# Kernel optimization log

Hardware: AMD Instinct MI355X
Metric: run time of the kernel (lower is better)

## Reference

```python
import jax, jax.numpy as jnp
import numpy as np

B, H, W, C = 32, 56, 56, 192
P, HEADS = 7, 6
HD = C // HEADS
SCALE = HD ** -0.5
EPS = 1e-5


def _rel_pos_index(p):
    coords = np.stack(np.meshgrid(np.arange(p), np.arange(p), indexing='ij')).reshape(2, -1)
    rel = (coords[:, :, None] - coords[:, None, :]).transpose(1, 2, 0).astype(np.int64)
    rel[:, :, 0] += p - 1
    rel[:, :, 1] += p - 1
    rel[:, :, 0] *= 2 * p - 1
    return rel.sum(-1)  # (p*p, p*p)

REL_IDX = jnp.asarray(_rel_pos_index(P))


def _ln(x, g, b):
    mu = x.mean(-1, keepdims=True)
    var = ((x - mu) ** 2).mean(-1, keepdims=True)
    return (x - mu) * jax.lax.rsqrt(var + EPS) * g + b


def setup_inputs():
    key = jax.random.key(0)
    ks = jax.random.split(key, 8)
    s = 0.02
    return {
        'x': jax.random.normal(ks[0], (B, H * W, C), jnp.float32),
        'norm1_g': jnp.ones((C,), jnp.float32),
        'norm1_b': jnp.zeros((C,), jnp.float32),
        'qkv_w': jax.random.normal(ks[1], (C, 3 * C), jnp.float32) * s,
        'qkv_b': jnp.zeros((3 * C,), jnp.float32),
        'rpe_table': jax.random.normal(ks[2], ((2 * P - 1) ** 2, HEADS), jnp.float32) * s,
        'proj_w': jax.random.normal(ks[3], (C, C), jnp.float32) * s,
        'proj_b': jnp.zeros((C,), jnp.float32),
        'norm2_g': jnp.ones((C,), jnp.float32),
        'norm2_b': jnp.zeros((C,), jnp.float32),
        'fc1_w': jax.random.normal(ks[4], (C, 4 * C), jnp.float32) * s,
        'fc1_b': jnp.zeros((4 * C,), jnp.float32),
        'fc2_w': jax.random.normal(ks[5], (4 * C, C), jnp.float32) * s,
        'fc2_b': jnp.zeros((C,), jnp.float32),
    }


def reference(x, norm1_g, norm1_b, qkv_w, qkv_b, rpe_table, proj_w, proj_b,
              norm2_g, norm2_b, fc1_w, fc1_b, fc2_w, fc2_b):
    N = P * P
    shortcut = x
    h = _ln(x, norm1_g, norm1_b).reshape(B, H, W, C)
    # partition -> (B*nH*nW, N, C)
    h = h.reshape(B, H // P, P, W // P, P, C).transpose(0, 1, 3, 2, 4, 5)
    patches = h.reshape(-1, N, C)
    B_ = patches.shape[0]
    # qkv
    qkv = (patches @ qkv_w + qkv_b).reshape(B_, N, 3, HEADS, HD)
    q, k, v = qkv[:, :, 0], qkv[:, :, 1], qkv[:, :, 2]  # (B_, N, HEADS, HD)
    attn = jnp.einsum('bnhd,bmhd->bhnm', q * SCALE, k)
    bias = rpe_table[REL_IDX.reshape(-1)].reshape(N, N, HEADS).transpose(2, 0, 1)
    attn = jax.nn.softmax(attn + bias[None], axis=-1)
    out = jnp.einsum('bhnm,bmhd->bnhd', attn, v).reshape(B_, N, C)
    out = out @ proj_w + proj_b
    # reverse -> (B, H*W, C)
    out = out.reshape(B, H // P, W // P, P, P, C).transpose(0, 1, 3, 2, 4, 5).reshape(B, H * W, C)
    x = shortcut + out
    h = _ln(x, norm2_g, norm2_b)
    h = jax.nn.gelu(h @ fc1_w + fc1_b, approximate=False) @ fc2_w + fc2_b
    return x + h
```

## Files before the change

kernel.cpp:

```cpp
#include <hip/hip_runtime.h>
#include <cstdint>

using u16 = unsigned short;
using u32 = unsigned int;

typedef __bf16 bf16x8 __attribute__((ext_vector_type(8)));
typedef float f32x4 __attribute__((ext_vector_type(4)));
typedef short short4v __attribute__((ext_vector_type(4)));

constexpr int TOK = 100352;
constexpr float LOG2E = 1.4426950408889634f;
constexpr float SCALE_QL = 0.25503490f;

__device__ __forceinline__ float bf2f(u16 u) {
  union { u32 i; float f; } z; z.i = ((u32)u) << 16; return z.f;
}
__device__ __forceinline__ u16 f2bf(float f) {
  union { float f; u32 i; } z; z.f = f;
  u32 r = z.i + 0x7FFFu + ((z.i >> 16) & 1u);
  return (u16)(r >> 16);
}
__device__ __forceinline__ u32 pk2bf(float a, float b) {
  union { __bf16 h[2]; u32 w; } z;
  z.h[0] = (__bf16)a; z.h[1] = (__bf16)b; return z.w;
}

__device__ __forceinline__ float gelu_f(float v) {
  float t = -v * (2.3022587f + 0.10294455f * v * v);
  float e = exp2f(t);
  return v * __builtin_amdgcn_rcpf(1.f + e);
}

__device__ __forceinline__ void gload_lds16(const void* g, void* l) {
  __builtin_amdgcn_global_load_lds((const __attribute__((address_space(1))) void*)g,
                                   (__attribute__((address_space(3))) void*)l, 16, 0, 0);
}

__global__ __launch_bounds__(256) void prep_weights(
    const float* __restrict__ qkv_w, const float* __restrict__ proj_w,
    const float* __restrict__ fc1_w, const float* __restrict__ fc2_w,
    u16* __restrict__ qkvT, u16* __restrict__ projT,
    u16* __restrict__ fc1T, u16* __restrict__ fc2T)
{
  int id = blockIdx.x * 256 + threadIdx.x;
  if (id < 122880) {
    int n = id / 192, k = id - n * 192;
    float v = (n < 576) ? qkv_w[(size_t)k * 576 + n] : 0.f;
    qkvT[id] = f2bf(v);
  } else if (id < 172032) {
    int t = id - 122880;
    int n = t / 192, k = t - n * 192;
    float v = (n < 192) ? proj_w[(size_t)k * 192 + n] : 0.f;
    projT[t] = f2bf(v);
  } else if (id < 319488) {
    int t = id - 172032;
    int n = t / 192, k = t - n * 192;
    int sg = (k >> 3) ^ (n & 7);
    fc1T[n * 192 + sg * 8 + (k & 7)] = f2bf(fc1_w[(size_t)k * 768 + n]);
  } else if (id < 466944) {
    int t = id - 319488;
    int oc = t / 768, gc = t - oc * 768;
    int ch = gc >> 5, gcl = gc & 31;
    int f = gcl >> 4, gq = (gcl >> 2) & 3, e = gcl & 3;
    int P = oc * 4 + (gq ^ ((oc >> 2) & 3));
    fc2T[ch * 6144 + P * 8 + f * 4 + e] = f2bf(fc2_w[(size_t)gc * 192 + oc]);
  }
}

__global__ __launch_bounds__(256) void ln_kernel(const float* __restrict__ x,
                                                 const float* __restrict__ g,
                                                 const float* __restrict__ b,
                                                 u16* __restrict__ out) {
  int row  = blockIdx.x * 4 + (threadIdx.x >> 6);
  int lane = threadIdx.x & 63;
  const float* xr = x + (size_t)row * 192;
  float v[3];
  #pragma unroll
  for (int t = 0; t < 3; ++t) v[t] = xr[lane + 64 * t];
  float s = v[0] + v[1] + v[2];
  #pragma unroll
  for (int o = 32; o; o >>= 1) s += __shfl_xor(s, o);
  float mu = s * (1.f / 192.f);
  float q = 0.f;
  #pragma unroll
  for (int t = 0; t < 3; ++t) { float d = v[t] - mu; q += d * d; }
  #pragma unroll
  for (int o = 32; o; o >>= 1) q += __shfl_xor(q, o);
  float rs = rsqrtf(q * (1.f / 192.f) + 1e-5f);
  #pragma unroll
  for (int t = 0; t < 3; ++t) {
    int c = lane + 64 * t;
    out[(size_t)row * 192 + c] = f2bf((v[t] - mu) * rs * g[c] + b[c]);
  }
}

enum { MQKV = 0 };

template<int MODE, int MT, int NT, int N, int K, int LDC>
__global__ __launch_bounds__(256) void gemm_kernel(
    const u16* __restrict__ A, const u16* __restrict__ BT,
    const float* __restrict__ bias,
    u16* __restrict__ outb)
{
  constexpr int NWG = MT * NT;
  constexpr int NTL = K / 32;
  __shared__ __align__(16) u16 As[3][4096];
  __shared__ __align__(16) u16 Bs[3][4096];
  int tid = threadIdx.x;
  int wg = blockIdx.x;
  int lin = (wg & 7) * (NWG / 8) + (wg >> 3);
  int tileM = (lin / NT) * 128, tileN = (lin % NT) * 128;
  int lane = tid & 63, wave = tid >> 6;
  int wm = wave >> 1, wn = wave & 1;
  int g = lane >> 4, l15 = lane & 15;
  f32x4 acc[4][4] = {};

  int r0 = tid >> 2, kc = (tid & 3) * 8;
  const u16* Arow0 = A  + (size_t)(tileM + r0)      * K + kc;
  const u16* Arow1 = A  + (size_t)(tileM + r0 + 64) * K + kc;
  const u16* Brow0 = BT + (size_t)(tileN + r0)      * K + kc;
  const u16* Brow1 = BT + (size_t)(tileN + r0 + 64) * K + kc;
  const int wo = wave * 512;

#define GSTAGE(buf, k0) do {                              \
    gload_lds16(Arow0 + (k0), &As[buf][wo]);              \
    gload_lds16(Arow1 + (k0), &As[buf][2048 + wo]);       \
    gload_lds16(Brow0 + (k0), &Bs[buf][wo]);              \
    gload_lds16(Brow1 + (k0), &Bs[buf][2048 + wo]);       \
  } while (0)

  GSTAGE(0, 0);
  GSTAGE(1, 32);

  #pragma unroll
  for (int t = 0; t < NTL; ++t) {
    if (t + 1 < NTL) asm volatile("s_waitcnt vmcnt(4)" ::: "memory");
    else             asm volatile("s_waitcnt vmcnt(0)" ::: "memory");
    __builtin_amdgcn_s_barrier();
    __builtin_amdgcn_sched_barrier(0);
    if (t + 2 < NTL) GSTAGE((t + 2) % 3, (t + 2) * 32);
    const int cur = t % 3;
    bf16x8 af[4], bfr[4];
    #pragma unroll
    for (int mi = 0; mi < 4; ++mi)
      af[mi] = *(const bf16x8*)&As[cur][(wm * 64 + mi * 16 + l15) * 32 + g * 8];
    #pragma unroll
    for (int ni = 0; ni < 4; ++ni)
      bfr[ni] = *(const bf16x8*)&Bs[cur][(wn * 64 + ni * 16 + l15) * 32 + g * 8];
    #pragma unroll
    for (int mi = 0; mi < 4; ++mi)
      #pragma unroll
      for (int ni = 0; ni < 4; ++ni)
        acc[mi][ni] = __builtin_amdgcn_mfma_f32_16x16x32_bf16(bfr[ni], af[mi], acc[mi][ni], 0, 0, 0);
    __builtin_amdgcn_sched_barrier(0);
  }
#undef GSTAGE

  int cb = tileN + wn * 64 + g * 4;
  f32x4 bv4[4];
  bool cok[4];
  #pragma unroll
  for (int ni = 0; ni < 4; ++ni) {
    cok[ni] = (cb + ni * 16) < N;
    bv4[ni] = cok[ni] ? *(const f32x4*)&bias[cb + ni * 16] : f32x4{};
  }
  #pragma unroll
  for (int mi = 0; mi < 4; ++mi) {
    size_t row = (size_t)(tileM + wm * 64 + mi * 16 + l15);
    u16* orow = outb + row * LDC + cb;
    #pragma unroll
    for (int ni = 0; ni < 4; ++ni) {
      if (!cok[ni]) continue;
      float v0 = acc[mi][ni][0] + bv4[ni][0];
      float v1 = acc[mi][ni][1] + bv4[ni][1];
      float v2 = acc[mi][ni][2] + bv4[ni][2];
      float v3 = acc[mi][ni][3] + bv4[ni][3];
      if (MODE == MQKV && (cb + ni * 16) < 192) {
        v0 *= SCALE_QL; v1 *= SCALE_QL; v2 *= SCALE_QL; v3 *= SCALE_QL;
      }
      uint2 w;
      w.x = pk2bf(v0, v1);
      w.y = pk2bf(v2, v3);
      *(uint2*)&orow[ni * 16] = w;
    }
  }
}

__global__ __launch_bounds__(256, 2) void proj_ln(
    const u16* __restrict__ A,
    const u16* __restrict__ BT,
    const float* __restrict__ bias,
    const float* __restrict__ x,
    const float* __restrict__ n2g, const float* __restrict__ n2b,
    float* __restrict__ resid, u16* __restrict__ h2)
{
  constexpr int NWG = 784;
  __shared__ __align__(16) u16 As[3][4096];
  __shared__ __align__(16) u16 Bs[3][6144];
  int tid = threadIdx.x;
  int wg = blockIdx.x;
  int lin = (wg & 7) * (NWG / 8) + (wg >> 3);
  int tileM = lin * 128;
  int lane = tid & 63, wave = tid >> 6;
  int g = lane >> 4, l15 = lane & 15;
  f32x4 acc[2][12] = {};

  int r0 = tid >> 2, kc = (tid & 3) * 8;
  const u16* Arow0 = A + (size_t)(tileM + r0)      * 192 + kc;
  const u16* Arow1 = A + (size_t)(tileM + r0 + 64) * 192 + kc;
  const u16* Brow[3];
  #pragma unroll
  for (int i = 0; i < 3; ++i) {
    int s = (wave * 3 + i) * 64 + lane;
    Brow[i] = BT + (size_t)(s >> 2) * 192 + (s & 3) * 8;
  }
  const int wo = wave * 512;

#define PSTAGE(buf, k0) do {                                   \
    gload_lds16(Arow0 + (k0), &As[buf][wo]);                   \
    gload_lds16(Arow1 + (k0), &As[buf][2048 + wo]);            \
    _Pragma("unroll")                                          \
    for (int i = 0; i < 3; ++i)                                \
      gload_lds16(Brow[i] + (k0), &Bs[buf][(wave * 3 + i) * 512]); \
  } while (0)

  PSTAGE(0, 0);
  PSTAGE(1, 32);

  #pragma unroll
  for (int t = 0; t < 6; ++t) {
    if (t + 1 < 6) asm volatile("s_waitcnt vmcnt(5)" ::: "memory");
    else           asm volatile("s_waitcnt vmcnt(0)" ::: "memory");
    __builtin_amdgcn_s_barrier();
    __builtin_amdgcn_sched_barrier(0);
    if (t + 2 < 6) PSTAGE((t + 2) % 3, (t + 2) * 32);
    const int cur = t % 3;
    bf16x8 af[2], bfr[12];
    #pragma unroll
    for (int mi = 0; mi < 2; ++mi)
      af[mi] = *(const bf16x8*)&As[cur][(wave * 32 + mi * 16 + l15) * 32 + g * 8];
    #pragma unroll
    for (int ni = 0; ni < 12; ++ni)
      bfr[ni] = *(const bf16x8*)&Bs[cur][(ni * 16 + l15) * 32 + g * 8];
    #pragma unroll
    for (int mi = 0; mi < 2; ++mi)
      #pragma unroll
      for (int ni = 0; ni < 12; ++ni)
        acc[mi][ni] = __builtin_amdgcn_mfma_f32_16x16x32_bf16(bfr[ni], af[mi], acc[mi][ni], 0, 0, 0);
    __builtin_amdgcn_sched_barrier(0);
  }
#undef PSTAGE

  float s1[2] = {0.f, 0.f}, s2[2] = {0.f, 0.f};
  #pragma unroll
  for (int mi = 0; mi < 2; ++mi) {
    size_t row = (size_t)(tileM + wave * 32 + mi * 16 + l15);
    #pragma unroll
    for (int ni = 0; ni < 12; ++ni) {
      int cb = ni * 16 + g * 4;
      f32x4 bv = *(const f32x4*)&bias[cb];
      f32x4 xv = *(const f32x4*)&x[row * 192 + cb];
      f32x4 o;
      #pragma unroll
      for (int r = 0; r < 4; ++r) {
        o[r] = acc[mi][ni][r] + bv[r] + xv[r];
        s1[mi] += o[r];
        s2[mi] += o[r] * o[r];
      }
      acc[mi][ni] = o;
      *(f32x4*)&resid[row * 192 + cb] = o;
    }
  }
  #pragma unroll
  for (int mi = 0; mi < 2; ++mi) {
    s1[mi] += __shfl_xor(s1[mi], 16); s1[mi] += __shfl_xor(s1[mi], 32);
    s2[mi] += __shfl_xor(s2[mi], 16); s2[mi] += __shfl_xor(s2[mi], 32);
  }
  #pragma unroll
  for (int mi = 0; mi < 2; ++mi) {
    float mu = s1[mi] * (1.f / 192.f);
    float var = s2[mi] * (1.f / 192.f) - mu * mu;
    float rs = rsqrtf(var + 1e-5f);
    size_t row = (size_t)(tileM + wave * 32 + mi * 16 + l15);
    #pragma unroll
    for (int ni = 0; ni < 12; ++ni) {
      int cb = ni * 16 + g * 4;
      f32x4 gv = *(const f32x4*)&n2g[cb];
      f32x4 bv = *(const f32x4*)&n2b[cb];
      uint2 w;
      w.x = pk2bf((acc[mi][ni][0] - mu) * rs * gv[0] + bv[0],
                  (acc[mi][ni][1] - mu) * rs * gv[1] + bv[1]);
      w.y = pk2bf((acc[mi][ni][2] - mu) * rs * gv[2] + bv[2],
                  (acc[mi][ni][3] - mu) * rs * gv[3] + bv[3]);
      *(uint2*)&h2[row * 192 + cb] = w;
    }
  }
}

__global__ __launch_bounds__(256, 3) void mlp_fused(
    const u16* __restrict__ h2, const float* __restrict__ resid,
    const u16* __restrict__ w1g,
    const u16* __restrict__ w2g,
    const float* __restrict__ fc1b, const float* __restrict__ fc2b,
    float* __restrict__ out)
{
  __shared__ __align__(16) u16 W1c[2][6144];
  __shared__ __align__(16) u16 W2c[2][6144];
  __shared__ float B1s[768];
  __shared__ float B2s[192];

  int tid = threadIdx.x, lane = tid & 63, wave = tid >> 6;
  int g = lane >> 4, l15 = lane & 15;
  size_t row = (size_t)blockIdx.x * 64 + wave * 16 + l15;

  for (int c = tid; c < 768; c += 256) B1s[c] = fc1b[c];
  if (tid < 192) B2s[tid] = fc2b[tid];

  bf16x8 xf[6];
  #pragma unroll
  for (int ks = 0; ks < 6; ++ks)
    xf[ks] = *(const bf16x8*)&h2[row * 192 + ks * 32 + g * 8];

#define MSTAGE(c) do {                                                    \
    _Pragma("unroll")                                                     \
    for (int it = 0; it < 3; ++it) {                                      \
      int s = it * 256 + tid;                                             \
      gload_lds16(w1g + (size_t)(c) * 6144 + s * 8,                       \
                  &W1c[(c) & 1][(it * 256 + wave * 64) * 8]);             \
      gload_lds16(w2g + (size_t)(c) * 6144 + s * 8,                       \
                  &W2c[(c) & 1][(it * 256 + wave * 64) * 8]);             \
    }                                                                     \
  } while (0)

  MSTAGE(0);
  __syncthreads();

  f32x4 accO[12] = {};
  const int p2sw = g ^ ((l15 >> 2) & 3);

  #pragma unroll 2
  for (int c = 0; c < 24; ++c) {
    asm volatile("s_waitcnt vmcnt(0)" ::: "memory");
    __builtin_amdgcn_s_barrier();
    __builtin_amdgcn_sched_barrier(0);
    if (c + 1 < 24) MSTAGE(c + 1);
    const int bs = c & 1;

    f32x4 acc1[2] = {};
    #pragma unroll
    for (int ks = 0; ks < 6; ++ks) {
      #pragma unroll
      for (int f = 0; f < 2; ++f) {
        int rl = f * 16 + l15;
        int sg = (ks * 4 + g) ^ (rl & 7);
        bf16x8 wf = *(const bf16x8*)&W1c[bs][rl * 192 + sg * 8];
        acc1[f] = __builtin_amdgcn_mfma_f32_16x16x32_bf16(wf, xf[ks], acc1[f], 0, 0, 0);
      }
    }
    short4v bp[2];
    #pragma unroll
    for (int f = 0; f < 2; ++f) {
      f32x4 bv = *(const f32x4*)&B1s[c * 32 + f * 16 + g * 4];
      float p0 = gelu_f(acc1[f][0] + bv[0]);
      float p1 = gelu_f(acc1[f][1] + bv[1]);
      float p2 = gelu_f(acc1[f][2] + bv[2]);
      float p3 = gelu_f(acc1[f][3] + bv[3]);
      union { u32 w[2]; short4v v; } uu;
      uu.w[0] = pk2bf(p0, p1);
      uu.w[1] = pk2bf(p2, p3);
      bp[f] = uu.v;
    }
    #pragma unroll
    for (int n = 0; n < 12; ++n) {
      int oc = n * 16 + l15;
      int P = oc * 4 + p2sw;
      union { bf16x8 v8; short4v h[2]; } wu;
      wu.v8 = *(const bf16x8*)&W2c[bs][P * 8];
      accO[n] = __builtin_amdgcn_mfma_f32_16x16x16bf16_1k(wu.h[0], bp[0], accO[n], 0, 0, 0);
      accO[n] = __builtin_amdgcn_mfma_f32_16x16x16bf16_1k(wu.h[1], bp[1], accO[n], 0, 0, 0);
    }
    __builtin_amdgcn_sched_barrier(0);
  }
#undef MSTAGE

  const float* rrow = resid + row * 192;
  float*      orow = out + row * 192;
  #pragma unroll
  for (int n = 0; n < 12; ++n) {
    int cb = n * 16 + g * 4;
    f32x4 bv = *(const f32x4*)&B2s[cb];
    f32x4 rv = *(const f32x4*)&rrow[cb];
    f32x4 o;
    o[0] = accO[n][0] + bv[0] + rv[0];
    o[1] = accO[n][1] + bv[1] + rv[1];
    o[2] = accO[n][2] + bv[2] + rv[2];
    o[3] = accO[n][3] + bv[3] + rv[3];
    *(f32x4*)&orow[cb] = o;
  }
}

__global__ __launch_bounds__(384, 4) void attn_kernel(const u16* __restrict__ qkv,
                                                      const float* __restrict__ rpe,
                                                      u16* __restrict__ aout) {
  __shared__ __align__(16) u16 VT[192 * 72];
  __shared__ float RPE[1014];

  int tid = threadIdx.x;
  int win = blockIdx.x;
  int b = win >> 6, rem = win & 63, wh = rem >> 3, ww = rem & 7;
  const size_t wbase = (size_t)b * 3136 + (size_t)(wh * 7) * 56 + ww * 7;

  for (int c = tid; c < 1176; c += 384) {
    int dchunk = c / 49, tkn = c - dchunk * 49;
    int d0 = dchunk * 8;
    int yi = tkn / 7, xi = tkn - yi * 7;
    size_t t = wbase + yi * 56 + xi;
    uint4 v = *(const uint4*)&qkv[t * 576 + 384 + d0];
    const u16* e = (const u16*)&v;
    #pragma unroll
    for (int u = 0; u < 8; ++u) VT[(d0 + u) * 72 + tkn] = e[u];
  }
  for (int c = tid; c < 2880; c += 384) {
    int d = c / 15, n = 49 + (c - d * 15);
    VT[d * 72 + n] = 0;
  }
  for (int c = tid; c < 1014; c += 384) RPE[c] = rpe[c] * LOG2E;
  __syncthreads();

  int wave = tid >> 6, lane = tid & 63;
  int g = lane >> 4, l15 = lane & 15;
  int h = wave;

  bf16x8 afk[4], bfq[4];
  #pragma unroll
  for (int f = 0; f < 4; ++f) {
    int row = f * 16 + l15; row = min(row, 48);
    int y = row / 7, xx = row - y * 7;
    const u16* base = &qkv[(wbase + (size_t)y * 56 + xx) * 576];
    bfq[f] = *(const bf16x8*)(base + h * 32 + g * 8);
    afk[f] = *(const bf16x8*)(base + 192 + h * 32 + g * 8);
  }

  f32x4 acc[4][4] = {};
  __builtin_amdgcn_s_setprio(1);
  #pragma unroll
  for (int mj = 0; mj < 4; ++mj)
    #pragma unroll
    for (int ni = 0; ni < 4; ++ni)
      acc[mj][ni] = __builtin_amdgcn_mfma_f32_16x16x32_bf16(afk[mj], bfq[ni], acc[mj][ni], 0, 0, 0);
  __builtin_amdgcn_s_setprio(0);

  float sums[4];
  short4v bp[4][4];
  #pragma unroll
  for (int ni = 0; ni < 4; ++ni) {
    int i = ni * 16 + l15;
    int yi = i / 7, xi = i - yi * 7;
    #pragma unroll
    for (int mj = 0; mj < 4; ++mj)
      #pragma unroll
      for (int r = 0; r < 4; ++r) {
        int j = mj * 16 + g * 4 + r;
        int yj = j / 7, xj = j - yj * 7;
        int idx = (yi - yj + 6) * 13 + (xi - xj + 6);
        idx = max(0, min(idx, 168));
        float s = acc[mj][ni][r] + RPE[idx * 6 + h];
        acc[mj][ni][r] = (j < 49) ? s : -1e30f;
      }
    float m = -1e30f;
    #pragma unroll
    for (int mj = 0; mj < 4; ++mj) {
      f32x4 a = acc[mj][ni];
      m = fmaxf(m, fmaxf(fmaxf(a[0], a[1]), fmaxf(a[2], a[3])));
    }
    m = fmaxf(m, __shfl_xor(m, 16));
    m = fmaxf(m, __shfl_xor(m, 32));
    float sum = 0.f;
    #pragma unroll
    for (int mj = 0; mj < 4; ++mj) {
      float p0 = exp2f(acc[mj][ni][0] - m);
      float p1 = exp2f(acc[mj][ni][1] - m);
      float p2 = exp2f(acc[mj][ni][2] - m);
      float p3 = exp2f(acc[mj][ni][3] - m);
      sum += (p0 + p1) + (p2 + p3);
      union { u32 w[2]; short4v v; } uu;
      uu.w[0] = pk2bf(p0, p1);
      uu.w[1] = pk2bf(p2, p3);
      bp[ni][mj] = uu.v;
    }
    sum += __shfl_xor(sum, 16);
    sum += __shfl_xor(sum, 32);
    sums[ni] = sum;
  }

  f32x4 accO[2][4] = {};
  #pragma unroll
  for (int ks = 0; ks < 4; ++ks) {
    short4v av[2];
    #pragma unroll
    for (int md = 0; md < 2; ++md)
      av[md] = *(const short4v*)&VT[(h * 32 + md * 16 + l15) * 72 + ks * 16 + g * 4];
    __builtin_amdgcn_s_setprio(1);
    #pragma unroll
    for (int md = 0; md < 2; ++md)
      #pragma unroll
      for (int ni = 0; ni < 4; ++ni)
        accO[md][ni] = __builtin_amdgcn_mfma_f32_16x16x16bf16_1k(av[md], bp[ni][ks], accO[md][ni], 0, 0, 0);
    __builtin_amdgcn_s_setprio(0);
  }

  #pragma unroll
  for (int ni = 0; ni < 4; ++ni) {
    int i = ni * 16 + l15;
    if (i >= 49) continue;
    float inv = __builtin_amdgcn_rcpf(sums[ni]);
    int y = i / 7, xx = i - y * 7;
    u16* orow = &aout[(wbase + (size_t)y * 56 + xx) * 192 + h * 32];
    #pragma unroll
    for (int md = 0; md < 2; ++md) {
      int d0 = md * 16 + g * 4;
      *(u32*)&orow[d0]     = pk2bf(accO[md][ni][0] * inv, accO[md][ni][1] * inv);
      *(u32*)&orow[d0 + 2] = pk2bf(accO[md][ni][2] * inv, accO[md][ni][3] * inv);
    }
  }
}

extern "C" void kernel_launch(void* const* d_in, const int* in_sizes, int n_in,
                              void* d_out, int out_size, void* d_ws, size_t ws_size,
                              hipStream_t stream) {
  const float* x      = (const float*)d_in[0];
  const float* n1g    = (const float*)d_in[1];
  const float* n1b    = (const float*)d_in[2];
  const float* qkv_w  = (const float*)d_in[3];
  const float* qkv_b  = (const float*)d_in[4];
  const float* rpe    = (const float*)d_in[5];
  const float* proj_w = (const float*)d_in[6];
  const float* proj_b = (const float*)d_in[7];
  const float* n2g    = (const float*)d_in[8];
  const float* n2b    = (const float*)d_in[9];
  const float* fc1_w  = (const float*)d_in[10];
  const float* fc1_b  = (const float*)d_in[11];
  const float* fc2_w  = (const float*)d_in[12];
  const float* fc2_b  = (const float*)d_in[13];
  float* out = (float*)d_out;
  char* ws = (char*)d_ws;

  u16* qkvT  = (u16*)(ws + 0);
  u16* projT = (u16*)(ws + 245760);
  u16* fc1T  = (u16*)(ws + 344064);
  u16* fc2T  = (u16*)(ws + 638976);
  u16* ln1   = (u16*)(ws + 1048576);
  u16* qkvB  = (u16*)(ws + 39583744);
  float* resid = (float*)(ws + 78118912);
  u16* attnO = ln1;
  u16* h2    = qkvB;
  if (ws_size < 193724416u) return;

  prep_weights<<<1824, 256, 0, stream>>>(qkv_w, proj_w, fc1_w, fc2_w,
                                         qkvT, projT, fc1T, fc2T);

  ln_kernel<<<TOK/4, 256, 0, stream>>>(x, n1g, n1b, ln1);

  gemm_kernel<MQKV, 784, 5, 576, 192, 576><<<3920, 256, 0, stream>>>(
      ln1, qkvT, qkv_b, qkvB);

  attn_kernel<<<2048, 384, 0, stream>>>(qkvB, rpe, attnO);

  proj_ln<<<784, 256, 0, stream>>>(
      attnO, projT, proj_b, x, n2g, n2b, resid, h2);

  mlp_fused<<<TOK/64, 256, 0, stream>>>(
      h2, resid, fc1T, fc2T, fc1_b, fc2_b, out);
}
```

Before: 332.9 us.

## Retile QKV GEMM to 128x64 tiles with full-K B resident and per-wave A pipelining

Replaces the generic 128x128 QKV GEMM with a specialized kernel using 128x64 output tiles (9 N-tiles exactly covering 576, so no padded waste like 5x128=640). The whole 64x192 weight slice is loaded into LDS once, and each wave streams its own 32-row A slice through a private triple buffer, so the per-k-step block barriers go away. This is meant to cut wasted MFMA work on padded columns and barrier stalls. In exchange it launches more workgroups and A tiles are re-read across 9 N-tiles instead of 5.

Result: slower. 351.1 us (+5.5%).

```diff
diff --git a/kernel.cpp b/kernel.cpp
--- a/kernel.cpp
+++ b/kernel.cpp
@@ -94,88 +94,83 @@
   }
 }
 
-enum { MQKV = 0 };
-
-template<int MODE, int MT, int NT, int N, int K, int LDC>
-__global__ __launch_bounds__(256) void gemm_kernel(
+__global__ __launch_bounds__(256) void qkv_kernel(
     const u16* __restrict__ A, const u16* __restrict__ BT,
     const float* __restrict__ bias,
     u16* __restrict__ outb)
 {
-  constexpr int NWG = MT * NT;
-  constexpr int NTL = K / 32;
-  __shared__ __align__(16) u16 As[3][4096];
-  __shared__ __align__(16) u16 Bs[3][4096];
+  constexpr int NWG = 7056;
+  __shared__ __align__(16) u16 LDS[24576];
+  u16* Bl = LDS + 12288;
+
   int tid = threadIdx.x;
   int wg = blockIdx.x;
   int lin = (wg & 7) * (NWG / 8) + (wg >> 3);
-  int tileM = (lin / NT) * 128, tileN = (lin % NT) * 128;
+  int tileM = (lin / 9) * 128, tileN = (lin % 9) * 64;
   int lane = tid & 63, wave = tid >> 6;
-  int wm = wave >> 1, wn = wave & 1;
   int g = lane >> 4, l15 = lane & 15;
-  f32x4 acc[4][4] = {};
-
-  int r0 = tid >> 2, kc = (tid & 3) * 8;
-  const u16* Arow0 = A  + (size_t)(tileM + r0)      * K + kc;
-  const u16* Arow1 = A  + (size_t)(tileM + r0 + 64) * K + kc;
-  const u16* Brow0 = BT + (size_t)(tileN + r0)      * K + kc;
-  const u16* Brow1 = BT + (size_t)(tileN + r0 + 64) * K + kc;
-  const int wo = wave * 512;
-
-#define GSTAGE(buf, k0) do {                              \
-    gload_lds16(Arow0 + (k0), &As[buf][wo]);              \
-    gload_lds16(Arow1 + (k0), &As[buf][2048 + wo]);       \
-    gload_lds16(Brow0 + (k0), &Bs[buf][wo]);              \
-    gload_lds16(Brow1 + (k0), &Bs[buf][2048 + wo]);       \
+  f32x4 acc[2][4] = {};
+
+  #pragma unroll
+  for (int rnd = 0; rnd < 6; ++rnd) {
+    int s = rnd * 256 + tid;
+    int c = s >> 6, n = s & 63;
+    gload_lds16(BT + (size_t)(tileN + n) * 192 + c * 8, &Bl[(rnd * 256 + wave * 64) * 8]);
+  }
+  const u16* Arow = A + (size_t)(tileM + wave * 32) * 192;
+#define ASTAGE(t) do {                                                        \
+    const int b_ = (t) % 3;                                                   \
+    _Pragma("unroll")                                                         \
+    for (int i_ = 0; i_ < 2; ++i_) {                                          \
+      int s_ = i_ * 64 + lane;                                                \
+      gload_lds16(Arow + (size_t)(s_ & 31) * 192 + (t) * 32 + (s_ >> 5) * 8,  \
+                  &LDS[((wave * 3 + b_) * 128 + i_ * 64) * 8]);               \
+    }                                                                         \
   } while (0)
 
-  GSTAGE(0, 0);
-  GSTAGE(1, 32);
-
-  #pragma unroll
-  for (int t = 0; t < NTL; ++t) {
-    if (t + 1 < NTL) asm volatile("s_waitcnt vmcnt(4)" ::: "memory");
-    else             asm volatile("s_waitcnt vmcnt(0)" ::: "memory");
-    __builtin_amdgcn_s_barrier();
+  ASTAGE(0);
+  ASTAGE(1);
+  __syncthreads();
+
+  int cb = tileN + g * 4;
+  f32x4 bv4[4];
+  #pragma unroll
+  for (int ni = 0; ni < 4; ++ni) bv4[ni] = *(const f32x4*)&bias[cb + ni * 16];
+
+  #pragma unroll
+  for (int t = 0; t < 6; ++t) {
+    if (t + 2 < 6) ASTAGE(t + 2);
+    if (t < 4)      asm volatile("s_waitcnt vmcnt(4)" ::: "memory");
+    else if (t == 4) asm volatile("s_waitcnt vmcnt(2)" ::: "memory");
+    else            asm volatile("s_waitcnt vmcnt(0)" ::: "memory");
     __builtin_amdgcn_sched_barrier(0);
-    if (t + 2 < NTL) GSTAGE((t + 2) % 3, (t + 2) * 32);
-    const int cur = t % 3;
-    bf16x8 af[4], bfr[4];
-    #pragma unroll
-    for (int mi = 0; mi < 4; ++mi)
-      af[mi] = *(const bf16x8*)&As[cur][(wm * 64 + mi * 16 + l15) * 32 + g * 8];
+    const int buf = t % 3;
+    bf16x8 af[2], bfr[4];
+    #pragma unroll
+    for (int mi = 0; mi < 2; ++mi)
+      af[mi] = *(const bf16x8*)&LDS[((wave * 3 + buf) * 128 + g * 32 + mi * 16 + l15) * 8];
     #pragma unroll
     for (int ni = 0; ni < 4; ++ni)
-      bfr[ni] = *(const bf16x8*)&Bs[cur][(wn * 64 + ni * 16 + l15) * 32 + g * 8];
-    #pragma unroll
-    for (int mi = 0; mi < 4; ++mi)
+      bfr[ni] = *(const bf16x8*)&Bl[((t * 4 + g) * 64 + ni * 16 + l15) * 8];
+    #pragma unroll
+    for (int mi = 0; mi < 2; ++mi)
       #pragma unroll
       for (int ni = 0; ni < 4; ++ni)
         acc[mi][ni] = __builtin_amdgcn_mfma_f32_16x16x32_bf16(bfr[ni], af[mi], acc[mi][ni], 0, 0, 0);
-    __builtin_amdgcn_sched_barrier(0);
-  }
-#undef GSTAGE
-
-  int cb = tileN + wn * 64 + g * 4;
-  f32x4 bv4[4];
-  bool cok[4];
-  #pragma unroll
-  for (int ni = 0; ni < 4; ++ni) {
-    cok[ni] = (cb + ni * 16) < N;
-    bv4[ni] = cok[ni] ? *(const f32x4*)&bias[cb + ni * 16] : f32x4{};
-  }
-  #pragma unroll
-  for (int mi = 0; mi < 4; ++mi) {
-    size_t row = (size_t)(tileM + wm * 64 + mi * 16 + l15);
-    u16* orow = outb + row * LDC + cb;
+  }
+#undef ASTAGE
+
+  #pragma unroll
+  for (int mi = 0; mi < 2; ++mi) {
+    size_t row = (size_t)(tileM + wave * 32 + mi * 16 + l15);
+    u16* orow = outb + row * 576 + cb;
     #pragma unroll
     for (int ni = 0; ni < 4; ++ni) {
-      if (!cok[ni]) continue;
       float v0 = acc[mi][ni][0] + bv4[ni][0];
       float v1 = acc[mi][ni][1] + bv4[ni][1];
       float v2 = acc[mi][ni][2] + bv4[ni][2];
       float v3 = acc[mi][ni][3] + bv4[ni][3];
-      if (MODE == MQKV && (cb + ni * 16) < 192) {
+      if ((cb + ni * 16) < 192) {
         v0 *= SCALE_QL; v1 *= SCALE_QL; v2 *= SCALE_QL; v3 *= SCALE_QL;
       }
       uint2 w;
@@ -561,8 +556,7 @@
 
   ln_kernel<<<TOK/4, 256, 0, stream>>>(x, n1g, n1b, ln1);
 
-  gemm_kernel<MQKV, 784, 5, 576, 192, 576><<<3920, 256, 0, stream>>>(
-      ln1, qkvT, qkv_b, qkvB);
+  qkv_kernel<<<7056, 256, 0, stream>>>(ln1, qkvT, qkv_b, qkvB);
 
   attn_kernel<<<2048, 384, 0, stream>>>(qkvB, rpe, attnO);
 
```
